# Optimization experiments

Hardware: AMD Instinct MI355X
Metric: run time of the kernel (lower is better)

## Reference

```python
import jax, jax.numpy as jnp
import numpy as np

N_HEADS = 16
HEAD_SIZE = 64

def setup_inputs() -> dict:
    key = jax.random.key(0)
    k1, k2 = jax.random.split(key)
    B, N, D = 2, 2048, N_HEADS * HEAD_SIZE
    x = jax.random.normal(k1, (B, N, D), dtype=jnp.float32)
    # lecun_normal-ish scale for the QKV kernel
    W_qkv = jax.random.normal(k2, (D, 3 * D), dtype=jnp.float32) * (1.0 / np.sqrt(D))
    return {"x": x, "W_qkv": W_qkv}

def reference(x, W_qkv):
    B, N, D = x.shape
    H, Dh = N_HEADS, HEAD_SIZE
    qkv = x @ W_qkv                                  # [B,N,3D]
    q, k, v = jnp.split(qkv, 3, axis=-1)
    q = q.reshape(B, N, H, Dh)
    k = k.reshape(B, N, H, Dh)
    v = v.reshape(B, N, H, Dh)
    dist = jnp.einsum('bihd,bjhd->bhij', q, k) / jnp.sqrt(jnp.asarray(Dh, dtype=x.dtype))
    mask = jnp.tril(jnp.ones((N, N), dtype=bool))[None, None, :, :]
    dist = jnp.where(mask, dist, -jnp.inf)
    attn = jax.nn.softmax(dist, axis=-1)             # [B,H,N,N]
    out_heads = jnp.einsum('bhij,bjhd->bihd', attn, v)
    return out_heads.reshape(B, N, H * Dh)
```

## Files before the change

kernel.cpp:

```cpp
#include <hip/hip_runtime.h>

typedef __attribute__((ext_vector_type(8))) short bf16x8;
typedef __attribute__((ext_vector_type(4))) float f32x4;

#define DEVI static __device__ __forceinline__

namespace {
constexpr int NSEQ = 2048, NH = 16;
constexpr int D = 1024, D3 = 3072;
}

DEVI unsigned short f2bf(float f) {
  union { float f; unsigned int u; } v; v.f = f;
  unsigned int r = v.u + 0x7FFFu + ((v.u >> 16) & 1u);
  return (unsigned short)(r >> 16);
}

DEVI void gload16(const unsigned short* g, unsigned short* lds) {
  __builtin_amdgcn_global_load_lds(
      (const __attribute__((address_space(1))) unsigned int*)g,
      (__attribute__((address_space(3))) unsigned int*)lds, 16, 0, 0);
}

DEVI f32x4 mfma16(bf16x8 a, bf16x8 b, f32x4 c) {
  return __builtin_amdgcn_mfma_f32_16x16x32_bf16(a, b, c, 0, 0, 0);
}

DEVI float exp2g(float x) {
#if __has_builtin(__builtin_amdgcn_exp2f)
  return __builtin_amdgcn_exp2f(x);
#else
  return exp2f(x);
#endif
}

DEVI unsigned int cvtpk(float a, float b) {
  unsigned int r;
  asm("v_cvt_pk_bf16_f32 %0, %1, %2" : "=v"(r) : "v"(a), "v"(b));
  return r;
}

__global__ __launch_bounds__(256) void prep_k(const float* __restrict__ x,
                                              const float* __restrict__ W,
                                              unsigned short* __restrict__ xb,
                                              unsigned short* __restrict__ Wt) {
  __shared__ float t[32][33];
  const int bid = blockIdx.x;
  if (bid < 4096) {
    int i = (bid * 256 + threadIdx.x) * 4;
    float4 v = *reinterpret_cast<const float4*>(x + i);
    ushort4 o;
    o.x = f2bf(v.x); o.y = f2bf(v.y); o.z = f2bf(v.z); o.w = f2bf(v.w);
    *reinterpret_cast<ushort4*>(xb + i) = o;
  } else {
    const int b2 = bid - 4096;
    const int c0 = (b2 % 96) * 32, k0 = (b2 / 96) * 32;
    const int tx = threadIdx.x & 31, ty = threadIdx.x >> 5;
#pragma unroll
    for (int r = 0; r < 32; r += 8)
      t[ty + r][tx] = W[(size_t)(k0 + ty + r) * D3 + c0 + tx];
    __syncthreads();
#pragma unroll
    for (int r = 0; r < 32; r += 8)
      Wt[(size_t)(c0 + ty + r) * D + k0 + tx] = f2bf(t[tx][ty + r]);
  }
}

__global__ __launch_bounds__(256) void qkv_gemm_k(const unsigned short* __restrict__ xb,
                                                  const unsigned short* __restrict__ Wt,
                                                  unsigned short* __restrict__ qw,
                                                  unsigned short* __restrict__ kw,
                                                  unsigned short* __restrict__ vtw) {
  __shared__ unsigned short smA[128 * 32];
  __shared__ unsigned short smB[128 * 32];
  const int tid = threadIdx.x, w = tid >> 6, l = tid & 63;
  const int m0 = blockIdx.x * 128, n0 = blockIdx.y * 128;
  const int wm = w >> 1, wn = w & 1;

  const unsigned short* ga[2]; const unsigned short* gb[2];
  unsigned short* la[2]; unsigned short* lb[2];
#pragma unroll
  for (int i = 0; i < 2; ++i) {
    int idx = tid + i * 256;
    int row = idx >> 2;
    int blk = (idx & 3) ^ ((row >> 1) & 3);
    ga[i] = xb + (size_t)(m0 + row) * D + blk * 8;
    gb[i] = Wt + (size_t)(n0 + row) * D + blk * 8;
    la[i] = smA + (w * 64 + i * 256) * 8;
    lb[i] = smB + (w * 64 + i * 256) * 8;
  }

  f32x4 acc[4][4];
#pragma unroll
  for (int a = 0; a < 4; ++a)
#pragma unroll
    for (int b = 0; b < 4; ++b) acc[a][b] = (f32x4){0.f, 0.f, 0.f, 0.f};

  for (int kt = 0; kt < D / 32; ++kt) {
    __syncthreads();
#pragma unroll
    for (int i = 0; i < 2; ++i) {
      gload16(ga[i] + kt * 32, la[i]);
      gload16(gb[i] + kt * 32, lb[i]);
    }
    asm volatile("s_waitcnt vmcnt(0)" ::: "memory");
    __syncthreads();

    bf16x8 af[4], bfr[4];
#pragma unroll
    for (int a = 0; a < 4; ++a) {
      int arow = wm * 64 + a * 16 + (l & 15);
      int blk = (l >> 4) ^ ((arow >> 1) & 3);
      af[a] = *reinterpret_cast<const bf16x8*>(smA + arow * 32 + blk * 8);
    }
#pragma unroll
    for (int b = 0; b < 4; ++b) {
      int brow = wn * 64 + b * 16 + (l & 15);
      int blk = (l >> 4) ^ ((brow >> 1) & 3);
      bfr[b] = *reinterpret_cast<const bf16x8*>(smB + brow * 32 + blk * 8);
    }
#pragma unroll
    for (int a = 0; a < 4; ++a)
#pragma unroll
      for (int b = 0; b < 4; ++b)
        acc[a][b] = mfma16(af[a], bfr[b], acc[a][b]);
  }

  const int which = n0 >> 10;
#pragma unroll
  for (int a = 0; a < 4; ++a) {
#pragma unroll
    for (int b = 0; b < 4; ++b) {
#pragma unroll
      for (int r = 0; r < 4; ++r) {
        int grow = m0 + wm * 64 + a * 16 + (l >> 4) * 4 + r;
        int gcol = n0 + wn * 64 + b * 16 + (l & 15);
        float v = acc[a][b][r];
        int bb = grow >> 11, n = grow & 2047;
        int cc = gcol & 1023, h = cc >> 6, dh = cc & 63;
        size_t bh = (size_t)bb * NH + h;
        if (which == 0)
          qw[(bh * NSEQ + n) * 64 + dh] = f2bf(v * 0.18033688011112042f);
        else if (which == 1)
          kw[(bh * NSEQ + n) * 64 + dh] = f2bf(v);
        else
          vtw[(bh * 64 + dh) * NSEQ + n] = f2bf(v);
      }
    }
  }
}

__global__ __launch_bounds__(256, 4) void attn_k(const unsigned short* __restrict__ qw,
                                                 const unsigned short* __restrict__ kw,
                                                 const unsigned short* __restrict__ vtw,
                                                 float* __restrict__ out) {
  __shared__ unsigned short smK[2][64 * 64];
  __shared__ unsigned short smV[2][64 * 64];
  __shared__ unsigned short smP[4][16 * 64];
  const int tid = threadIdx.x, w = tid >> 6, l = tid & 63;
  const int g = l >> 4, ql = l & 15;
  const int qx = (ql & 7) << 4;

  const int wg = blockIdx.x;
  const int xcd = wg & 7, rest = wg >> 3;
  const int bhl = rest >> 4;
  const int j = rest & 15;
  const int bh = xcd * 4 + bhl;
  const int b = bh >> 4, h = bh & 15;

  const unsigned short* qb = qw + (size_t)bh * NSEQ * 64;
  const unsigned short* kb = kw + (size_t)bh * NSEQ * 64;
  const unsigned short* vb = vtw + (size_t)bh * 64 * NSEQ;
  char* pl = (char*)smP[w];

  const int i0 = tid, i1 = tid + 256;
  const int r0 = i0 >> 3, c0 = (i0 & 7) ^ (r0 & 7);
  const int r1 = i1 >> 3, c1 = (i1 & 7) ^ (r1 & 7);

#define STAGE(B, T)                                                               \
  do {                                                                            \
    gload16(kb + ((size_t)(T) * 64 + r0) * 64 + c0 * 8, smK[B] + w * 512);        \
    gload16(vb + (size_t)r0 * NSEQ + (T) * 64 + c0 * 8, smV[B] + w * 512);        \
    gload16(kb + ((size_t)(T) * 64 + r1) * 64 + c1 * 8, smK[B] + w * 512 + 2048); \
    gload16(vb + (size_t)r1 * NSEQ + (T) * 64 + c1 * 8, smV[B] + w * 512 + 2048); \
  } while (0)

  for (int seg = 0; seg < 2; ++seg) {
    const int qt = seg ? j : (31 - j);
    const int qbase = qt * 64;

    const int qrow = qbase + w * 16 + ql;
    const bf16x8 qf0 = *reinterpret_cast<const bf16x8*>(qb + (size_t)qrow * 64 + g * 8);
    const bf16x8 qf1 = *reinterpret_cast<const bf16x8*>(qb + (size_t)qrow * 64 + 32 + g * 8);

    float m = -1e30f, lsum = 0.f;
    f32x4 o[4];
#pragma unroll
    for (int c = 0; c < 4; ++c) o[c] = (f32x4){0.f, 0.f, 0.f, 0.f};

    STAGE(0, 0);
    for (int t = 0; t <= qt; ++t) {
      __syncthreads();
      const int cur = t & 1;
      if (t < qt) STAGE(cur ^ 1, t + 1);

      const unsigned short* K = smK[cur];
      const unsigned short* V = smV[cur];

      f32x4 sc4[4];
#pragma unroll
      for (int c = 0; c < 4; ++c) sc4[c] = (f32x4){0.f, 0.f, 0.f, 0.f};
      __builtin_amdgcn_s_setprio(1);
#pragma unroll
      for (int c = 0; c < 4; ++c) {
        const int krow = c * 16 + ql, sw = krow & 7;
        bf16x8 kf0 = *reinterpret_cast<const bf16x8*>(K + krow * 64 + ((g ^ sw) * 8));
        bf16x8 kf1 = *reinterpret_cast<const bf16x8*>(K + krow * 64 + (((4 + g) ^ sw) * 8));
        sc4[c] = mfma16(kf0, qf0, sc4[c]);
        sc4[c] = mfma16(kf1, qf1, sc4[c]);
      }
      __builtin_amdgcn_s_setprio(0);

      if (t == qt) {
        const int qloc = w * 16 + ql;
#pragma unroll
        for (int c = 0; c < 4; ++c)
#pragma unroll
          for (int r = 0; r < 4; ++r)
            if (c * 16 + g * 4 + r > qloc) sc4[c][r] = -1e30f;
      }

      float tmax = sc4[0][0];
#pragma unroll
      for (int c = 0; c < 4; ++c)
#pragma unroll
        for (int r = 0; r < 4; ++r) tmax = fmaxf(tmax, sc4[c][r]);
      tmax = fmaxf(tmax, __shfl_xor(tmax, 16, 64));
      tmax = fmaxf(tmax, __shfl_xor(tmax, 32, 64));

      if (!__all(tmax <= m + 8.0f)) {
        const float mn = fmaxf(m, tmax);
        const float sc = exp2g(m - mn);
        m = mn;
        lsum *= sc;
        float sco[4];
#pragma unroll
        for (int r = 0; r < 4; ++r) sco[r] = __shfl(sc, (l & 48) + g * 4 + r, 64);
#pragma unroll
        for (int c = 0; c < 4; ++c)
#pragma unroll
          for (int r = 0; r < 4; ++r) o[c][r] *= sco[r];
      }

      float rsum = 0.f;
#pragma unroll
      for (int c = 0; c < 4; ++c) {
        float p0 = exp2g(sc4[c][0] - m), p1 = exp2g(sc4[c][1] - m);
        float p2 = exp2g(sc4[c][2] - m), p3 = exp2g(sc4[c][3] - m);
        rsum += (p0 + p1) + (p2 + p3);
        unsigned int u0 = cvtpk(p0, p1), u1 = cvtpk(p2, p3);
        *reinterpret_cast<uint2*>(pl + ql * 128 + ((32 * c + 8 * g) ^ qx)) =
            make_uint2(u0, u1);
      }
      rsum += __shfl_xor(rsum, 16, 64);
      rsum += __shfl_xor(rsum, 32, 64);
      lsum += rsum;

      asm volatile("s_waitcnt lgkmcnt(0)" ::: "memory");
      __builtin_amdgcn_sched_barrier(0);

      bf16x8 pf0 = *reinterpret_cast<const bf16x8*>(pl + ql * 128 + ((16 * g) ^ qx));
      bf16x8 pf1 = *reinterpret_cast<const bf16x8*>(pl + ql * 128 + ((64 + 16 * g) ^ qx));
      __builtin_amdgcn_s_setprio(1);
#pragma unroll
      for (int c = 0; c < 4; ++c) {
        const int vrow = c * 16 + ql, sw = vrow & 7;
        bf16x8 vf0 = *reinterpret_cast<const bf16x8*>(V + vrow * 64 + ((g ^ sw) * 8));
        bf16x8 vf1 = *reinterpret_cast<const bf16x8*>(V + vrow * 64 + (((4 + g) ^ sw) * 8));
        o[c] = mfma16(pf0, vf0, o[c]);
        o[c] = mfma16(pf1, vf1, o[c]);
      }
      __builtin_amdgcn_s_setprio(0);
    }

    const float linv = 1.0f / lsum;
    float lo4[4];
#pragma unroll
    for (int r = 0; r < 4; ++r) lo4[r] = __shfl(linv, (l & 48) + g * 4 + r, 64);
#pragma unroll
    for (int c = 0; c < 4; ++c) {
#pragma unroll
      for (int r = 0; r < 4; ++r) {
        const int n = qbase + w * 16 + g * 4 + r;
        const int dh = c * 16 + ql;
        out[((size_t)b * NSEQ + n) * D + h * 64 + dh] = o[c][r] * lo4[r];
      }
    }
    __syncthreads();
  }
#undef STAGE
}

extern "C" void kernel_launch(void* const* d_in, const int* in_sizes, int n_in,
                              void* d_out, int out_size, void* d_ws, size_t ws_size,
                              hipStream_t stream) {
  const float* x = (const float*)d_in[0];
  const float* W = (const float*)d_in[1];
  float* out = (float*)d_out;
  char* ws = (char*)d_ws;
  unsigned short* xb  = (unsigned short*)(ws);
  unsigned short* Wt  = (unsigned short*)(ws + 8388608);
  unsigned short* qw  = (unsigned short*)(ws + 14680064);
  unsigned short* kw  = (unsigned short*)(ws + 23068672);
  unsigned short* vtw = (unsigned short*)(ws + 31457280);

  prep_k<<<7168, 256, 0, stream>>>(x, W, xb, Wt);
  qkv_gemm_k<<<dim3(32, 24), 256, 0, stream>>>(xb, Wt, qw, kw, vtw);
  attn_k<<<512, 256, 0, stream>>>(qw, kw, vtw, out);
}
```

Before: 89.95 us.

## Triple-buffer K/V tiles and software-pipeline next QK^T MFMA over softmax

The attention inner loop moves from double to triple buffering of K/V tiles in LDS and prefetches two tiles ahead. The QK^T MFMA cluster for the next tile is issued before the PV MFMAs of the current tile, so its matrix work can overlap with the softmax and exp work. This is meant to hide global load latency and keep the matrix units busy. In exchange it uses more LDS (which may lower occupancy under launch_bounds 4), holds more live registers for the extra score fragments, and keeps one block-wide barrier per iteration, now placed at a different point.

```diff
diff --git a/kernel.cpp b/kernel.cpp
--- a/kernel.cpp
+++ b/kernel.cpp
@@ -154,8 +154,8 @@
                                                  const unsigned short* __restrict__ kw,
                                                  const unsigned short* __restrict__ vtw,
                                                  float* __restrict__ out) {
-  __shared__ unsigned short smK[2][64 * 64];
-  __shared__ unsigned short smV[2][64 * 64];
+  __shared__ unsigned short smK[3][64 * 64];
+  __shared__ unsigned short smV[3][64 * 64];
   __shared__ unsigned short smP[4][16 * 64];
   const int tid = threadIdx.x, w = tid >> 6, l = tid & 63;
   const int g = l >> 4, ql = l & 15;
@@ -185,6 +185,23 @@
     gload16(vb + (size_t)r1 * NSEQ + (T) * 64 + c1 * 8, smV[B] + w * 512 + 2048); \
   } while (0)
 
+#define QK_CLUSTER(KBUF, DST)                                                     \
+  do {                                                                            \
+    _Pragma("unroll") for (int c_ = 0; c_ < 4; ++c_)                              \
+        DST[c_] = (f32x4){0.f, 0.f, 0.f, 0.f};                                    \
+    __builtin_amdgcn_s_setprio(1);                                                \
+    _Pragma("unroll") for (int c_ = 0; c_ < 4; ++c_) {                            \
+      const int krow_ = c_ * 16 + ql, sw_ = krow_ & 7;                            \
+      bf16x8 kf0_ = *reinterpret_cast<const bf16x8*>((KBUF) + krow_ * 64 +        \
+                                                     ((g ^ sw_) * 8));            \
+      bf16x8 kf1_ = *reinterpret_cast<const bf16x8*>((KBUF) + krow_ * 64 +        \
+                                                     (((4 + g) ^ sw_) * 8));      \
+      DST[c_] = mfma16(kf0_, qf0, DST[c_]);                                       \
+      DST[c_] = mfma16(kf1_, qf1, DST[c_]);                                       \
+    }                                                                             \
+    __builtin_amdgcn_s_setprio(0);                                                \
+  } while (0)
+
   for (int seg = 0; seg < 2; ++seg) {
     const int qt = seg ? j : (31 - j);
     const int qbase = qt * 64;
@@ -199,42 +216,28 @@
     for (int c = 0; c < 4; ++c) o[c] = (f32x4){0.f, 0.f, 0.f, 0.f};
 
     STAGE(0, 0);
+    if (qt >= 1) STAGE(1, 1);
+    __syncthreads();
+
+    f32x4 scur[4], snext[4];
+    QK_CLUSTER(smK[0], scur);
+
+    int s0 = 0, s1 = 1, s2 = 2;
     for (int t = 0; t <= qt; ++t) {
-      __syncthreads();
-      const int cur = t & 1;
-      if (t < qt) STAGE(cur ^ 1, t + 1);
-
-      const unsigned short* K = smK[cur];
-      const unsigned short* V = smV[cur];
-
-      f32x4 sc4[4];
-#pragma unroll
-      for (int c = 0; c < 4; ++c) sc4[c] = (f32x4){0.f, 0.f, 0.f, 0.f};
-      __builtin_amdgcn_s_setprio(1);
-#pragma unroll
-      for (int c = 0; c < 4; ++c) {
-        const int krow = c * 16 + ql, sw = krow & 7;
-        bf16x8 kf0 = *reinterpret_cast<const bf16x8*>(K + krow * 64 + ((g ^ sw) * 8));
-        bf16x8 kf1 = *reinterpret_cast<const bf16x8*>(K + krow * 64 + (((4 + g) ^ sw) * 8));
-        sc4[c] = mfma16(kf0, qf0, sc4[c]);
-        sc4[c] = mfma16(kf1, qf1, sc4[c]);
-      }
-      __builtin_amdgcn_s_setprio(0);
-
       if (t == qt) {
         const int qloc = w * 16 + ql;
 #pragma unroll
         for (int c = 0; c < 4; ++c)
 #pragma unroll
           for (int r = 0; r < 4; ++r)
-            if (c * 16 + g * 4 + r > qloc) sc4[c][r] = -1e30f;
-      }
-
-      float tmax = sc4[0][0];
+            if (c * 16 + g * 4 + r > qloc) scur[c][r] = -1e30f;
+      }
+
+      float tmax = scur[0][0];
 #pragma unroll
       for (int c = 0; c < 4; ++c)
 #pragma unroll
-        for (int r = 0; r < 4; ++r) tmax = fmaxf(tmax, sc4[c][r]);
+        for (int r = 0; r < 4; ++r) tmax = fmaxf(tmax, scur[c][r]);
       tmax = fmaxf(tmax, __shfl_xor(tmax, 16, 64));
       tmax = fmaxf(tmax, __shfl_xor(tmax, 32, 64));
 
@@ -255,8 +258,8 @@
       float rsum = 0.f;
 #pragma unroll
       for (int c = 0; c < 4; ++c) {
-        float p0 = exp2g(sc4[c][0] - m), p1 = exp2g(sc4[c][1] - m);
-        float p2 = exp2g(sc4[c][2] - m), p3 = exp2g(sc4[c][3] - m);
+        float p0 = exp2g(scur[c][0] - m), p1 = exp2g(scur[c][1] - m);
+        float p2 = exp2g(scur[c][2] - m), p3 = exp2g(scur[c][3] - m);
         rsum += (p0 + p1) + (p2 + p3);
         unsigned int u0 = cvtpk(p0, p1), u1 = cvtpk(p2, p3);
         *reinterpret_cast<uint2*>(pl + ql * 128 + ((32 * c + 8 * g) ^ qx)) =
@@ -266,9 +269,15 @@
       rsum += __shfl_xor(rsum, 32, 64);
       lsum += rsum;
 
+      __syncthreads();
+
+      if (t + 2 <= qt) STAGE(s2, t + 2);
+      if (t + 1 <= qt) QK_CLUSTER(smK[s1], snext);
+
       asm volatile("s_waitcnt lgkmcnt(0)" ::: "memory");
       __builtin_amdgcn_sched_barrier(0);
 
+      const unsigned short* V = smV[s0];
       bf16x8 pf0 = *reinterpret_cast<const bf16x8*>(pl + ql * 128 + ((16 * g) ^ qx));
       bf16x8 pf1 = *reinterpret_cast<const bf16x8*>(pl + ql * 128 + ((64 + 16 * g) ^ qx));
       __builtin_amdgcn_s_setprio(1);
@@ -281,6 +290,12 @@
         o[c] = mfma16(pf1, vf1, o[c]);
       }
       __builtin_amdgcn_s_setprio(0);
+
+      if (t < qt) {
+#pragma unroll
+        for (int c = 0; c < 4; ++c) scur[c] = snext[c];
+      }
+      const int tmp = s0; s0 = s1; s1 = s2; s2 = tmp;
     }
 
     const float linv = 1.0f / lsum;
@@ -299,6 +314,7 @@
     __syncthreads();
   }
 #undef STAGE
+#undef QK_CLUSTER
 }
 
 extern "C" void kernel_launch(void* const* d_in, const int* in_sizes, int n_in,
```

Measured after the change: 92.03 us. 2.3% more time.

## Rewrite attention loop with 32x32 MFMA and split-KV across wave pairs

Applied to the files above, without the earlier changes.

The attention kernel switches from 16x16x32 to 32x32x16 bf16 MFMA, with each wave handling 32 query rows. Wave pairs split alternate key tiles, so two K/V tiles are staged per iteration, and their partial softmax states are merged through LDS at the end. P is moved between lanes with permlane32_swap instead of an LDS round trip, and the output is written with coalesced float4 stores. In exchange, the kernel uses about 65KB of LDS, which lowers occupancy to 2 blocks per CU, and it adds a merge step with extra barriers.

```diff
diff --git a/kernel.cpp b/kernel.cpp
--- a/kernel.cpp
+++ b/kernel.cpp
@@ -2,6 +2,8 @@
 
 typedef __attribute__((ext_vector_type(8))) short bf16x8;
 typedef __attribute__((ext_vector_type(4))) float f32x4;
+typedef __attribute__((ext_vector_type(16))) float f32x16;
+typedef __attribute__((ext_vector_type(2))) unsigned int u32x2;
 
 #define DEVI static __device__ __forceinline__
 
@@ -16,14 +18,18 @@
   return (unsigned short)(r >> 16);
 }
 
-DEVI void gload16(const unsigned short* g, unsigned short* lds) {
+DEVI void gload16(const unsigned short* g, unsigned short* lds_) {
   __builtin_amdgcn_global_load_lds(
       (const __attribute__((address_space(1))) unsigned int*)g,
-      (__attribute__((address_space(3))) unsigned int*)lds, 16, 0, 0);
+      (__attribute__((address_space(3))) unsigned int*)lds_, 16, 0, 0);
 }
 
 DEVI f32x4 mfma16(bf16x8 a, bf16x8 b, f32x4 c) {
   return __builtin_amdgcn_mfma_f32_16x16x32_bf16(a, b, c, 0, 0, 0);
+}
+
+DEVI f32x16 mfma32(bf16x8 a, bf16x8 b, f32x16 c) {
+  return __builtin_amdgcn_mfma_f32_32x32x16_bf16(a, b, c, 0, 0, 0);
 }
 
 DEVI float exp2g(float x) {
@@ -39,6 +45,24 @@
   asm("v_cvt_pk_bf16_f32 %0, %1, %2" : "=v"(r) : "v"(a), "v"(b));
   return r;
 }
+
+DEVI u32x2 pswap2(unsigned int a, unsigned int b) {
+  return __builtin_amdgcn_permlane32_swap(a, b, false, false);
+}
+DEVI float xmax_halves(float v) {
+  union { float f; unsigned int u; } c; c.f = v;
+  u32x2 r = pswap2(c.u, c.u);
+  union { unsigned int u; float f; } x, y; x.u = r.x; y.u = r.y;
+  return fmaxf(x.f, y.f);
+}
+DEVI float xsum_halves(float v) {
+  union { float f; unsigned int u; } c; c.f = v;
+  u32x2 r = pswap2(c.u, c.u);
+  union { unsigned int u; float f; } x, y; x.u = r.x; y.u = r.y;
+  return x.f + y.f;
+}
+
+union U4 { unsigned int u[4]; bf16x8 v; };
 
 __global__ __launch_bounds__(256) void prep_k(const float* __restrict__ x,
                                               const float* __restrict__ W,
@@ -150,150 +174,201 @@
   }
 }
 
-__global__ __launch_bounds__(256, 4) void attn_k(const unsigned short* __restrict__ qw,
+__global__ __launch_bounds__(256, 2) void attn_k(const unsigned short* __restrict__ qw,
                                                  const unsigned short* __restrict__ kw,
                                                  const unsigned short* __restrict__ vtw,
                                                  float* __restrict__ out) {
-  __shared__ unsigned short smK[2][64 * 64];
-  __shared__ unsigned short smV[2][64 * 64];
-  __shared__ unsigned short smP[4][16 * 64];
+  __shared__ __align__(16) char lds[66560];
   const int tid = threadIdx.x, w = tid >> 6, l = tid & 63;
-  const int g = l >> 4, ql = l & 15;
-  const int qx = (ql & 7) << 4;
+  const int hi = l >> 5, ql = l & 31;
+  const int qsub = w >> 1, par = w & 1;
 
   const int wg = blockIdx.x;
   const int xcd = wg & 7, rest = wg >> 3;
   const int bhl = rest >> 4;
   const int j = rest & 15;
   const int bh = xcd * 4 + bhl;
-  const int b = bh >> 4, h = bh & 15;
+  const int bb = bh >> 4, h = bh & 15;
 
   const unsigned short* qb = qw + (size_t)bh * NSEQ * 64;
   const unsigned short* kb = kw + (size_t)bh * NSEQ * 64;
   const unsigned short* vb = vtw + (size_t)bh * 64 * NSEQ;
-  char* pl = (char*)smP[w];
-
-  const int i0 = tid, i1 = tid + 256;
-  const int r0 = i0 >> 3, c0 = (i0 & 7) ^ (r0 & 7);
-  const int r1 = i1 >> 3, c1 = (i1 & 7) ^ (r1 & 7);
-
-#define STAGE(B, T)                                                               \
-  do {                                                                            \
-    gload16(kb + ((size_t)(T) * 64 + r0) * 64 + c0 * 8, smK[B] + w * 512);        \
-    gload16(vb + (size_t)r0 * NSEQ + (T) * 64 + c0 * 8, smV[B] + w * 512);        \
-    gload16(kb + ((size_t)(T) * 64 + r1) * 64 + c1 * 8, smK[B] + w * 512 + 2048); \
-    gload16(vb + (size_t)r1 * NSEQ + (T) * 64 + c1 * 8, smV[B] + w * 512 + 2048); \
+
+  const int r0 = tid >> 3, c0 = (tid & 7) ^ (r0 & 7);
+  const int r1 = (tid + 256) >> 3, c1 = ((tid + 256) & 7) ^ (r1 & 7);
+  const int wbase = w * 512;
+
+#define STAGE(SL, PR)                                                            \
+  do {                                                                           \
+    const int t0_ = 2 * (PR), t1_ = 2 * (PR) + 1;                                \
+    unsigned short* k0d = (unsigned short*)(lds + (SL) * 32768) + wbase;         \
+    unsigned short* v0d = (unsigned short*)(lds + (SL) * 32768 + 8192) + wbase;  \
+    unsigned short* k1d = (unsigned short*)(lds + (SL) * 32768 + 16384) + wbase; \
+    unsigned short* v1d = (unsigned short*)(lds + (SL) * 32768 + 24576) + wbase; \
+    gload16(kb + (((size_t)t0_ * 64 + r0) * 64 + c0 * 8), k0d);                  \
+    gload16(kb + (((size_t)t0_ * 64 + r1) * 64 + c1 * 8), k0d + 2048);           \
+    gload16(vb + ((size_t)r0 * NSEQ + t0_ * 64 + c0 * 8), v0d);                  \
+    gload16(vb + ((size_t)r1 * NSEQ + t0_ * 64 + c1 * 8), v0d + 2048);           \
+    gload16(kb + (((size_t)t1_ * 64 + r0) * 64 + c0 * 8), k1d);                  \
+    gload16(kb + (((size_t)t1_ * 64 + r1) * 64 + c1 * 8), k1d + 2048);           \
+    gload16(vb + ((size_t)r0 * NSEQ + t1_ * 64 + c0 * 8), v1d);                  \
+    gload16(vb + ((size_t)r1 * NSEQ + t1_ * 64 + c1 * 8), v1d + 2048);           \
   } while (0)
 
   for (int seg = 0; seg < 2; ++seg) {
     const int qt = seg ? j : (31 - j);
     const int qbase = qt * 64;
-
-    const int qrow = qbase + w * 16 + ql;
-    const bf16x8 qf0 = *reinterpret_cast<const bf16x8*>(qb + (size_t)qrow * 64 + g * 8);
-    const bf16x8 qf1 = *reinterpret_cast<const bf16x8*>(qb + (size_t)qrow * 64 + 32 + g * 8);
+    const int qg = qbase + qsub * 32 + ql;
+
+    bf16x8 qf[4];
+#pragma unroll
+    for (int ds = 0; ds < 4; ++ds)
+      qf[ds] = *reinterpret_cast<const bf16x8*>(qb + (size_t)qg * 64 + ds * 16 + hi * 8);
 
     float m = -1e30f, lsum = 0.f;
-    f32x4 o[4];
-#pragma unroll
-    for (int c = 0; c < 4; ++c) o[c] = (f32x4){0.f, 0.f, 0.f, 0.f};
-
+    f32x16 O0, O1;
+#pragma unroll
+    for (int r2 = 0; r2 < 16; ++r2) { O0[r2] = 0.f; O1[r2] = 0.f; }
+
+    const int nsup = (qt >> 1) + 1;
     STAGE(0, 0);
-    for (int t = 0; t <= qt; ++t) {
+    for (int s = 0; s < nsup; ++s) {
       __syncthreads();
-      const int cur = t & 1;
-      if (t < qt) STAGE(cur ^ 1, t + 1);
-
-      const unsigned short* K = smK[cur];
-      const unsigned short* V = smV[cur];
-
-      f32x4 sc4[4];
-#pragma unroll
-      for (int c = 0; c < 4; ++c) sc4[c] = (f32x4){0.f, 0.f, 0.f, 0.f};
-      __builtin_amdgcn_s_setprio(1);
+      if (s + 1 < nsup) STAGE((s + 1) & 1, s + 1);
+      const int t = 2 * s + par;
+      if (t <= qt) {
+        const char* Kb = lds + (s & 1) * 32768 + par * 16384;
+        const char* Vb = Kb + 8192;
+
+        f32x16 S0, S1;
+#pragma unroll
+        for (int r2 = 0; r2 < 16; ++r2) { S0[r2] = 0.f; S1[r2] = 0.f; }
+        __builtin_amdgcn_s_setprio(1);
+#pragma unroll
+        for (int ds = 0; ds < 4; ++ds) {
+          bf16x8 k0 = *reinterpret_cast<const bf16x8*>(
+              Kb + ql * 128 + (((2 * ds + hi) ^ (ql & 7)) << 4));
+          bf16x8 k1 = *reinterpret_cast<const bf16x8*>(
+              Kb + (32 + ql) * 128 + (((2 * ds + hi) ^ (ql & 7)) << 4));
+          S0 = mfma32(k0, qf[ds], S0);
+          S1 = mfma32(k1, qf[ds], S1);
+        }
+        __builtin_amdgcn_s_setprio(0);
+
+        if (t == qt) {
+#pragma unroll
+          for (int reg = 0; reg < 16; ++reg) {
+            const int krow = (reg & 3) + 8 * (reg >> 2) + 4 * hi;
+            if (64 * t + krow > qg) S0[reg] = -1e30f;
+            if (64 * t + 32 + krow > qg) S1[reg] = -1e30f;
+          }
+        }
+
+        float t0 = fmaxf(S0[0], S1[0]), t1 = fmaxf(S0[1], S1[1]);
+        float t2 = fmaxf(S0[2], S1[2]), t3 = fmaxf(S0[3], S1[3]);
+#pragma unroll
+        for (int r2 = 4; r2 < 16; r2 += 4) {
+          t0 = fmaxf(t0, fmaxf(S0[r2], S1[r2]));
+          t1 = fmaxf(t1, fmaxf(S0[r2 + 1], S1[r2 + 1]));
+          t2 = fmaxf(t2, fmaxf(S0[r2 + 2], S1[r2 + 2]));
+          t3 = fmaxf(t3, fmaxf(S0[r2 + 3], S1[r2 + 3]));
+        }
+        float tmax = xmax_halves(fmaxf(fmaxf(t0, t1), fmaxf(t2, t3)));
+
+        if (!__all(tmax <= m + 8.0f)) {
+          const float mn = fmaxf(m, tmax);
+          const float g = exp2g(m - mn);
+          m = mn;
+          lsum *= g;
+#pragma unroll
+          for (int r2 = 0; r2 < 16; ++r2) { O0[r2] *= g; O1[r2] *= g; }
+        }
+
+        float pr0[16], pr1[16];
+        float rA = 0.f, rB = 0.f, rC = 0.f, rD = 0.f;
+#pragma unroll
+        for (int r2 = 0; r2 < 16; r2 += 4) {
+          pr0[r2] = exp2g(S0[r2] - m);     pr1[r2] = exp2g(S1[r2] - m);
+          pr0[r2 + 1] = exp2g(S0[r2 + 1] - m); pr1[r2 + 1] = exp2g(S1[r2 + 1] - m);
+          pr0[r2 + 2] = exp2g(S0[r2 + 2] - m); pr1[r2 + 2] = exp2g(S1[r2 + 2] - m);
+          pr0[r2 + 3] = exp2g(S0[r2 + 3] - m); pr1[r2 + 3] = exp2g(S1[r2 + 3] - m);
+          rA += pr0[r2] + pr1[r2];
+          rB += pr0[r2 + 1] + pr1[r2 + 1];
+          rC += pr0[r2 + 2] + pr1[r2 + 2];
+          rD += pr0[r2 + 3] + pr1[r2 + 3];
+        }
+        lsum += xsum_halves((rA + rB) + (rC + rD));
+
+        bf16x8 pf[4];
+#pragma unroll
+        for (int ct = 0; ct < 2; ++ct) {
+          const float* pp = ct ? pr1 : pr0;
+          unsigned int u[4][2];
+#pragma unroll
+          for (int c = 0; c < 4; ++c) {
+            u[c][0] = cvtpk(pp[4 * c], pp[4 * c + 1]);
+            u[c][1] = cvtpk(pp[4 * c + 2], pp[4 * c + 3]);
+          }
+#pragma unroll
+          for (int kk = 0; kk < 2; ++kk) {
+            u32x2 rw0 = pswap2(u[2 * kk][0], u[2 * kk + 1][0]);
+            u32x2 rw1 = pswap2(u[2 * kk][1], u[2 * kk + 1][1]);
+            U4 f;
+            f.u[0] = rw0.x; f.u[1] = rw1.x;
+            f.u[2] = rw0.y; f.u[3] = rw1.y;
+            pf[2 * ct + kk] = f.v;
+          }
+        }
+
+        __builtin_amdgcn_s_setprio(1);
+#pragma unroll
+        for (int ks = 0; ks < 4; ++ks) {
+          bf16x8 v0 = *reinterpret_cast<const bf16x8*>(
+              Vb + ql * 128 + (((2 * ks + hi) ^ (ql & 7)) << 4));
+          bf16x8 v1 = *reinterpret_cast<const bf16x8*>(
+              Vb + (32 + ql) * 128 + (((2 * ks + hi) ^ (ql & 7)) << 4));
+          O0 = mfma32(v0, pf[ks], O0);
+          O1 = mfma32(v1, pf[ks], O1);
+        }
+        __builtin_amdgcn_s_setprio(0);
+      }
+    }
+
+    __syncthreads();
+    float* mlp = (float*)(lds + 65536);
+    if (l < 32) { mlp[w * 64 + l] = m; mlp[w * 64 + 32 + l] = lsum; }
+    __syncthreads();
+    {
+      const int pw = w ^ 1;
+      const float m1 = mlp[pw * 64 + ql];
+      const float l1 = mlp[pw * 64 + 32 + ql];
+      const float M = fmaxf(m, m1);
+      const float g0 = exp2g(m - M);
+      const float g1 = exp2g(m1 - M);
+      const float L = lsum * g0 + l1 * g1;
+      const float phi = g0 / L;
+      float* mo = (float*)lds + (qsub * 2 + par) * 2048;
+#pragma unroll
+      for (int reg = 0; reg < 16; ++reg) {
+        const int dr = (reg & 3) + 8 * (reg >> 2) + 4 * hi;
+        const int d1 = 32 + dr;
+        mo[ql * 64 + (((dr >> 2) ^ (ql & 7)) << 2) + (dr & 3)] = O0[reg] * phi;
+        mo[ql * 64 + (((d1 >> 2) ^ (ql & 7)) << 2) + (d1 & 3)] = O1[reg] * phi;
+      }
+    }
+    __syncthreads();
+    {
+      const int qq = tid >> 2, dq = (tid & 3) << 4;
+      const float* pa = (float*)lds + ((qq >> 5) * 2 + 0) * 2048 + (qq & 31) * 64;
+      const float* pb = (float*)lds + ((qq >> 5) * 2 + 1) * 2048 + (qq & 31) * 64;
+      float* op = out + ((size_t)bb * NSEQ + qbase + qq) * D + h * 64 + dq;
 #pragma unroll
       for (int c = 0; c < 4; ++c) {
-        const int krow = c * 16 + ql, sw = krow & 7;
-        bf16x8 kf0 = *reinterpret_cast<const bf16x8*>(K + krow * 64 + ((g ^ sw) * 8));
-        bf16x8 kf1 = *reinterpret_cast<const bf16x8*>(K + krow * 64 + (((4 + g) ^ sw) * 8));
-        sc4[c] = mfma16(kf0, qf0, sc4[c]);
-        sc4[c] = mfma16(kf1, qf1, sc4[c]);
-      }
-      __builtin_amdgcn_s_setprio(0);
-
-      if (t == qt) {
-        const int qloc = w * 16 + ql;
-#pragma unroll
-        for (int c = 0; c < 4; ++c)
-#pragma unroll
-          for (int r = 0; r < 4; ++r)
-            if (c * 16 + g * 4 + r > qloc) sc4[c][r] = -1e30f;
-      }
-
-      float tmax = sc4[0][0];
-#pragma unroll
-      for (int c = 0; c < 4; ++c)
-#pragma unroll
-        for (int r = 0; r < 4; ++r) tmax = fmaxf(tmax, sc4[c][r]);
-      tmax = fmaxf(tmax, __shfl_xor(tmax, 16, 64));
-      tmax = fmaxf(tmax, __shfl_xor(tmax, 32, 64));
-
-      if (!__all(tmax <= m + 8.0f)) {
-        const float mn = fmaxf(m, tmax);
-        const float sc = exp2g(m - mn);
-        m = mn;
-        lsum *= sc;
-        float sco[4];
-#pragma unroll
-        for (int r = 0; r < 4; ++r) sco[r] = __shfl(sc, (l & 48) + g * 4 + r, 64);
-#pragma unroll
-        for (int c = 0; c < 4; ++c)
-#pragma unroll
-          for (int r = 0; r < 4; ++r) o[c][r] *= sco[r];
-      }
-
-      float rsum = 0.f;
-#pragma unroll
-      for (int c = 0; c < 4; ++c) {
-        float p0 = exp2g(sc4[c][0] - m), p1 = exp2g(sc4[c][1] - m);
-        float p2 = exp2g(sc4[c][2] - m), p3 = exp2g(sc4[c][3] - m);
-        rsum += (p0 + p1) + (p2 + p3);
-        unsigned int u0 = cvtpk(p0, p1), u1 = cvtpk(p2, p3);
-        *reinterpret_cast<uint2*>(pl + ql * 128 + ((32 * c + 8 * g) ^ qx)) =
-            make_uint2(u0, u1);
-      }
-      rsum += __shfl_xor(rsum, 16, 64);
-      rsum += __shfl_xor(rsum, 32, 64);
-      lsum += rsum;
-
-      asm volatile("s_waitcnt lgkmcnt(0)" ::: "memory");
-      __builtin_amdgcn_sched_barrier(0);
-
-      bf16x8 pf0 = *reinterpret_cast<const bf16x8*>(pl + ql * 128 + ((16 * g) ^ qx));
-      bf16x8 pf1 = *reinterpret_cast<const bf16x8*>(pl + ql * 128 + ((64 + 16 * g) ^ qx));
-      __builtin_amdgcn_s_setprio(1);
-#pragma unroll
-      for (int c = 0; c < 4; ++c) {
-        const int vrow = c * 16 + ql, sw = vrow & 7;
-        bf16x8 vf0 = *reinterpret_cast<const bf16x8*>(V + vrow * 64 + ((g ^ sw) * 8));
-        bf16x8 vf1 = *reinterpret_cast<const bf16x8*>(V + vrow * 64 + (((4 + g) ^ sw) * 8));
-        o[c] = mfma16(pf0, vf0, o[c]);
-        o[c] = mfma16(pf1, vf1, o[c]);
-      }
-      __builtin_amdgcn_s_setprio(0);
-    }
-
-    const float linv = 1.0f / lsum;
-    float lo4[4];
-#pragma unroll
-    for (int r = 0; r < 4; ++r) lo4[r] = __shfl(linv, (l & 48) + g * 4 + r, 64);
-#pragma unroll
-    for (int c = 0; c < 4; ++c) {
-#pragma unroll
-      for (int r = 0; r < 4; ++r) {
-        const int n = qbase + w * 16 + g * 4 + r;
-        const int dh = c * 16 + ql;
-        out[((size_t)b * NSEQ + n) * D + h * 64 + dh] = o[c][r] * lo4[r];
+        const int ch = ((dq >> 2) + c) ^ (qq & 7);
+        float4 va = *reinterpret_cast<const float4*>(pa + ch * 4);
+        float4 vb4 = *reinterpret_cast<const float4*>(pb + ch * 4);
+        float4 s4 = make_float4(va.x + vb4.x, va.y + vb4.y, va.z + vb4.z, va.w + vb4.w);
+        *reinterpret_cast<float4*>(op + c * 4) = s4;
       }
     }
     __syncthreads();
```

Result: faster. 85.09 us (-5.4%).
